# Performance work log

Measured on AMD Instinct MI355X. Metric: run time of the kernel, lower is better.

The kernel has to match this reference:

```python
import jax, jax.numpy as jnp
import numpy as np

B, T = 128, 100
NOISE_STD = 0.1  # deterministic=False path

def leaky(x, slope):
    return jnp.where(x >= 0, x, slope * x)

def setup_inputs() -> dict:
    key = jax.random.key(0)
    ks = jax.random.split(key, 24)
    s = 0.02
    d = {}
    d["input_data"] = jax.random.normal(ks[0], (B, T, 3, 3), jnp.float32)
    d["eps"] = jax.random.normal(ks[1], (B, 64), jnp.float32)
    d["noise_eps"] = jax.random.normal(ks[2], (T, B, 4), jnp.float32)
    d["proj_W"] = jax.random.normal(ks[3], (4096, 9), jnp.float32) * s
    d["proj_b"] = jnp.zeros((4096,), jnp.float32)
    d["lstm_Wih"] = jax.random.normal(ks[4], (512, 4096), jnp.float32) * s
    d["lstm_Whh"] = jax.random.normal(ks[5], (512, 128), jnp.float32) * s
    d["lstm_bih"] = jnp.zeros((512,), jnp.float32)
    d["lstm_bhh"] = jnp.zeros((512,), jnp.float32)
    d["mu_W"] = jax.random.normal(ks[6], (64, 128), jnp.float32) * s
    d["mu_b"] = jnp.zeros((64,), jnp.float32)
    d["lv_W"] = jax.random.normal(ks[7], (64, 128), jnp.float32) * s
    d["lv_b"] = jnp.zeros((64,), jnp.float32)
    d["fcin_W"] = jax.random.normal(ks[8], (256, 64), jnp.float32) * s
    d["fcin_b"] = jnp.zeros((256,), jnp.float32)
    d["gru_Wih"] = jax.random.normal(ks[9], (783, 261), jnp.float32) * s
    d["gru_Whh"] = jax.random.normal(ks[10], (783, 261), jnp.float32) * s
    d["gru_bih"] = jnp.zeros((783,), jnp.float32)
    d["gru_bhh"] = jnp.zeros((783,), jnp.float32)
    d["jf_W1"] = jax.random.normal(ks[11], (64, 261), jnp.float32) * s
    d["jf_b1"] = jnp.zeros((64,), jnp.float32)
    d["jf_W2"] = jax.random.normal(ks[12], (9, 64), jnp.float32) * s
    d["jf_b2"] = jnp.zeros((9,), jnp.float32)
    return d

def reference(input_data, eps, noise_eps, proj_W, proj_b, lstm_Wih, lstm_Whh,
              lstm_bih, lstm_bhh, mu_W, mu_b, lv_W, lv_b, fcin_W, fcin_b,
              gru_Wih, gru_Whh, gru_bih, gru_bhh, jf_W1, jf_b1, jf_W2, jf_b2):
    b, t = input_data.shape[0], input_data.shape[1]
    pose = input_data.reshape(b, t, 9)
    # pose_projection: Linear(9, 4096) + LeakyReLU(0.1)
    proj = leaky(jnp.einsum('btj,kj->btk', pose, proj_W) + proj_b, 0.1)  # (B,T,4096)

    # LSTM over time, take final hidden state. PyTorch gate order: i,f,g,o.
    # Precompute input projections for all steps.
    x_gates = jnp.einsum('btk,gk->tbg', proj, lstm_Wih) + lstm_bih + lstm_bhh  # (T,B,512)
    hdim = 128
    def lstm_step(carry, xg):
        h, c = carry
        g = xg + h @ lstm_Whh.T  # (B,512)
        i, f, gg, o = jnp.split(g, 4, axis=-1)
        i, f, o = jax.nn.sigmoid(i), jax.nn.sigmoid(f), jax.nn.sigmoid(o)
        c = f * c + i * jnp.tanh(gg)
        h = o * jnp.tanh(c)
        return (h, c), None
    h0 = jnp.zeros((b, hdim), proj.dtype)
    (h_T, _), _ = jax.lax.scan(lstm_step, (h0, h0), x_gates)

    # VAE head (dropout in eval mode = identity)
    mu = leaky(h_T @ mu_W.T + mu_b, 0.1)
    logvar = jnp.clip(leaky(h_T @ lv_W.T + lv_b, 0.1), -10.0, 10.0)
    std = jnp.exp(0.5 * logvar)
    embedding = mu + eps * std

    x = embedding @ fcin_W.T + fcin_b  # (B,256)

    # Decoder GRU loop. PyTorch gate order: r,z,n; h' = (1-z)*n + z*h.
    noise = noise_eps * NOISE_STD  # (T,B,4)
    time_steps = (jnp.arange(t, dtype=x.dtype) / (t - 1))[:, None, None] * jnp.ones((t, b, 1), x.dtype)
    inp_seq = jnp.concatenate([jnp.broadcast_to(x[None], (t, b, 256)), noise, time_steps], axis=-1)  # (T,B,261)
    gx_seq = jnp.einsum('tbk,gk->tbg', inp_seq, gru_Wih) + gru_bih  # (T,B,783)

    def gru_step(h, gx):
        gh = h @ gru_Whh.T + gru_bhh
        gx_r, gx_z, gx_n = jnp.split(gx, 3, axis=-1)
        gh_r, gh_z, gh_n = jnp.split(gh, 3, axis=-1)
        r = jax.nn.sigmoid(gx_r + gh_r)
        z = jax.nn.sigmoid(gx_z + gh_z)
        n = jnp.tanh(gx_n + r * gh_n)
        h = (1.0 - z) * n + z * h
        frame = jax.nn.sigmoid(leaky(h @ jf_W1.T + jf_b1, 0.2) @ jf_W2.T + jf_b2)
        return h, frame

    h0g = jnp.zeros((b, 261), x.dtype)
    _, frames = jax.lax.scan(gru_step, h0g, gx_seq)  # (T,B,9)
    outputs = frames.transpose(1, 0, 2).reshape(b, t, 3, 3)
    return outputs, mu, logvar
```

## Files before the change

kernel.cpp:

```cpp
#include <hip/hip_runtime.h>
#include <hip/hip_bf16.h>

typedef float f32x4 __attribute__((ext_vector_type(4)));
typedef short s16x8 __attribute__((ext_vector_type(8)));

__device__ __forceinline__ float pv_sigm(float x){ return 1.0f/(1.0f + __expf(-x)); }
__device__ __forceinline__ float pv_tanh(float x){ float e = __expf(2.0f*x); return 1.0f - 2.0f/(e + 1.0f); }

__device__ __forceinline__ unsigned short pv_f2b(float x){
  union { float f; unsigned u; } c; c.f = x;
  unsigned r = (c.u + 0x7fffu + ((c.u >> 16) & 1u)) >> 16;
  return (unsigned short)r;
}
__device__ __forceinline__ unsigned pv_pack2(float a, float b){
  return ((unsigned)pv_f2b(b) << 16) | (unsigned)pv_f2b(a);
}
__device__ __forceinline__ float pv_lo(unsigned u){
  union { unsigned u; float f; } c; c.u = u << 16; return c.f;
}
__device__ __forceinline__ float pv_hi(unsigned u){
  union { unsigned u; float f; } c; c.u = u & 0xffff0000u; return c.f;
}

__device__ __forceinline__ unsigned char pv_fp8(float x){
  union { float f; unsigned u; } c; c.f = x;
  unsigned s = (c.u >> 24) & 0x80u;
  unsigned au = c.u & 0x7fffffffu;
  if (au == 0u) return (unsigned char)s;
  int ex = (int)(au >> 23) - 127;
  if (ex < -6) ex = -6;
  union { unsigned u; float f; } iv; iv.u = (unsigned)(3 - ex + 127) << 23;
  union { unsigned u; float f; } a;  a.u = au;
  int q = (int)rintf(a.f * iv.f);
  if (q >= 16) { q >>= 1; ex += 1; }
  unsigned bits;
  if (ex == -6 && q < 8) bits = (unsigned)q;
  else bits = (unsigned)(((ex + 7) << 3) | (q - 8));
  return (unsigned char)(s | bits);
}

#if defined(__has_builtin)
#if __has_builtin(__builtin_amdgcn_cvt_pk_fp8_f32)
#define PV_HW_FP8 1
#endif
#endif
__device__ __forceinline__ unsigned char pv_fp8_fast(float x){
#ifdef PV_HW_FP8
  return (unsigned char)__builtin_amdgcn_cvt_pk_fp8_f32(x, x, 0, false);
#else
  return pv_fp8(x);
#endif
}

__global__ void pv_prep_gru8(const float* Whh, const float* Wih,
                             unsigned long long* wfp8){
  int idx = blockIdx.x*256 + threadIdx.x;
  if (idx >= 29376) return;
  int T = idx / 576;
  int rem = idx - T*576;
  int c = rem >> 6;
  int l = rem & 63;
  int l16 = l & 15;
  int quad = l >> 4;
  int jb = T / 3;
  int ty = T - jb*3;
  int j = jb*16 + l16;
  int g = ty*261 + j;
  unsigned long long v = 0ull;
  #pragma unroll
  for (int e = 0; e < 8; ++e) {
    int k = c*32 + quad*8 + e;
    float w = 0.0f;
    if (j < 261) {
      if (k < 261) w = Whh[g*261 + k];
      else if (k < 266 && ty < 2) w = Wih[g*261 + 256 + (k - 261)];
    }
    v |= (unsigned long long)pv_fp8(8.0f*w) << (8*e);
  }
  wfp8[idx] = v;
}

__global__ __launch_bounds__(256) void pv_prep_wih(
    const float* __restrict__ Wih, unsigned* __restrict__ wihb)
{
  const int idx = blockIdx.x*256 + threadIdx.x;
  if (idx >= 262144) return;
  const float* src = Wih + idx*8;
  float4 a = *(const float4*)(src);
  float4 b = *(const float4*)(src + 4);
  uint4 o;
  o.x = pv_pack2(a.x, a.y);
  o.y = pv_pack2(a.z, a.w);
  o.z = pv_pack2(b.x, b.y);
  o.w = pv_pack2(b.z, b.w);
  *(uint4*)(wihb + idx*4) = o;
}

__global__ __launch_bounds__(512, 1) void pv_gemm4(
    const float* __restrict__ pose, const float* __restrict__ projW,
    const float* __restrict__ projb, const unsigned* __restrict__ wihb,
    const float* __restrict__ bih, const float* __restrict__ bhh,
    float* __restrict__ xg)
{
  __shared__ __align__(16) unsigned As2[128*20];
  __shared__ __align__(16) unsigned Bs2[2][256*20];
  __shared__ __align__(16) float Ws2[2][320];

  const int tid = threadIdx.x;
  const int m0 = blockIdx.x * 128;
  const int n0 = blockIdx.y * 256;
  const int wave = tid >> 6, lane = tid & 63;
  const int wm = wave >> 2, wn = wave & 3;
  const int l16 = lane & 15, quad = lane >> 4;
  const int rl = tid >> 2, kq = tid & 3;
  const int rb = tid >> 1, hb = tid & 1;

  float p[9];
  {
    const float* pr = pose + (m0 + rl)*9;
    #pragma unroll
    for (int j = 0; j < 9; ++j) p[j] = pr[j];
  }

  if (tid < 320) {
    Ws2[0][tid < 288 ? ((tid >> 5)*32 + (tid & 31)) : tid] =
        (tid < 288) ? projW[(tid & 31)*9 + (tid >> 5)] : projb[tid - 288];
  }
  {
    const unsigned* src = wihb + (n0 + rb)*2048 + hb*8;
    *(uint4*)(&Bs2[0][rb*20 + hb*8])     = *(const uint4*)(src);
    *(uint4*)(&Bs2[0][rb*20 + hb*8 + 4]) = *(const uint4*)(src + 4);
  }
  __syncthreads();

  f32x4 acc[4][4];
  #pragma unroll
  for (int i = 0; i < 4; ++i)
    #pragma unroll
    for (int j = 0; j < 4; ++j) acc[i][j] = (f32x4){0.f,0.f,0.f,0.f};

  for (int kk = 0; kk < 128; ++kk) {
    const int cur = kk & 1, nxt = cur ^ 1;
    const int kn = kk + 1;

    uint4 bn0, bn1; float wv = 0.0f;
    if (kn < 128) {
      const unsigned* bsrc = wihb + (n0 + rb)*2048 + kn*16 + hb*8;
      bn0 = *(const uint4*)(bsrc);
      bn1 = *(const uint4*)(bsrc + 4);
      if (tid < 320)
        wv = (tid < 288) ? projW[kn*288 + (tid & 31)*9 + (tid >> 5)]
                         : projb[kn*32 + (tid - 288)];
    }

    {
      const float* W = Ws2[cur];
      f32x4 slo = *(const f32x4*)(W + 288 + kq*8);
      f32x4 shi = *(const f32x4*)(W + 292 + kq*8);
      #pragma unroll
      for (int j = 0; j < 9; ++j) {
        f32x4 wlo = *(const f32x4*)(W + j*32 + kq*8);
        f32x4 whi = *(const f32x4*)(W + j*32 + kq*8 + 4);
        slo += p[j]*wlo;
        shi += p[j]*whi;
      }
      #pragma unroll
      for (int e = 0; e < 4; ++e) {
        slo[e] = fmaxf(slo[e], 0.1f*slo[e]);
        shi[e] = fmaxf(shi[e], 0.1f*shi[e]);
      }
      uint4 av;
      av.x = pv_pack2(slo[0], slo[1]);
      av.y = pv_pack2(slo[2], slo[3]);
      av.z = pv_pack2(shi[0], shi[1]);
      av.w = pv_pack2(shi[2], shi[3]);
      *(uint4*)(&As2[rl*20 + kq*4]) = av;
    }
    __syncthreads();

    {
      const unsigned short* As16 = (const unsigned short*)As2;
      const unsigned short* Bs16 = (const unsigned short*)Bs2[cur];
      s16x8 af[4];
      #pragma unroll
      for (int i = 0; i < 4; ++i)
        af[i] = *(const s16x8*)(As16 + (wm*64 + i*16 + l16)*40 + quad*8);
      #pragma unroll
      for (int j = 0; j < 4; ++j) {
        s16x8 bv = *(const s16x8*)(Bs16 + (wn*64 + j*16 + l16)*40 + quad*8);
        #pragma unroll
        for (int i = 0; i < 4; ++i)
          acc[i][j] = __builtin_amdgcn_mfma_f32_16x16x32_bf16(af[i], bv, acc[i][j], 0, 0, 0);
      }
    }

    if (kn < 128) {
      *(uint4*)(&Bs2[nxt][rb*20 + hb*8])     = bn0;
      *(uint4*)(&Bs2[nxt][rb*20 + hb*8 + 4]) = bn1;
      if (tid < 320)
        Ws2[nxt][tid < 288 ? ((tid >> 5)*32 + (tid & 31)) : tid] = wv;
    }
    __syncthreads();
  }

  #pragma unroll
  for (int j = 0; j < 4; ++j) {
    int col = n0 + wn*64 + j*16 + l16;
    float bsum = bih[col] + bhh[col];
    #pragma unroll
    for (int i = 0; i < 4; ++i) {
      #pragma unroll
      for (int r = 0; r < 4; ++r) {
        int row = m0 + wm*64 + i*16 + quad*4 + r;
        int bb = row / 100;
        int tt = row - bb*100;
        xg[(tt*128 + bb)*512 + col] = acc[i][j][r] + bsum;
      }
    }
  }
}

__global__ __launch_bounds__(256) void pv_gemm(
    const float* pose, const float* projW, const float* projb,
    const float* Wih, const float* bih, const float* bhh,
    float* xg)
{
  __shared__ __align__(16) unsigned As[128*24];
  __shared__ __align__(16) unsigned Bs[128*24];
  __shared__ float Ws[320];

  const int tid = threadIdx.x;
  const int m0 = blockIdx.x * 128;
  const int n0 = blockIdx.y * 128;

  const int rl = tid >> 1;
  const int kh = tid & 1;
  float p0,p1,p2,p3,p4,p5,p6,p7,p8;
  {
    const float* pr = pose + (m0 + rl) * 9;
    p0=pr[0]; p1=pr[1]; p2=pr[2]; p3=pr[3]; p4=pr[4];
    p5=pr[5]; p6=pr[6]; p7=pr[7]; p8=pr[8];
  }

  const int wave = tid >> 6;
  const int lane = tid & 63;
  const int wm = wave >> 1, wn = wave & 1;
  const int l16 = lane & 15, quad = lane >> 4;

  f32x4 acc[4][4];
  #pragma unroll
  for (int i = 0; i < 4; ++i)
    #pragma unroll
    for (int j = 0; j < 4; ++j) acc[i][j] = (f32x4){0.f,0.f,0.f,0.f};

  for (int kk = 0; kk < 128; ++kk) {
    __syncthreads();
    for (int idx = tid; idx < 320; idx += 256)
      Ws[idx] = (idx < 288) ? projW[kk*288 + idx] : projb[kk*32 + (idx - 288)];
    #pragma unroll
    for (int i = 0; i < 8; ++i) {
      int q = tid + i*256;
      int nl = q >> 4;
      int kp = q & 15;
      const float* src = Wih + (n0 + nl)*4096 + kk*32 + kp*2;
      Bs[nl*24 + kp] = pv_pack2(src[0], src[1]);
    }
    __syncthreads();
    {
      const int kbase = kh*16;
      const float* wbase = Ws + kbase*9;
      float av[16];
      #pragma unroll
      for (int u = 0; u < 16; ++u) {
        const float* wr = wbase + u*9;
        float s = Ws[288 + kbase + u]
                + p0*wr[0] + p1*wr[1] + p2*wr[2] + p3*wr[3] + p4*wr[4]
                + p5*wr[5] + p6*wr[6] + p7*wr[7] + p8*wr[8];
        av[u] = fmaxf(s, 0.1f*s);
      }
      #pragma unroll
      for (int q = 0; q < 8; ++q)
        As[rl*24 + kh*8 + q] = pv_pack2(av[2*q], av[2*q+1]);
    }
    __syncthreads();
    const unsigned short* As16 = (const unsigned short*)As;
    const unsigned short* Bs16 = (const unsigned short*)Bs;
    s16x8 af[4], bfv[4];
    #pragma unroll
    for (int i = 0; i < 4; ++i)
      af[i] = *(const s16x8*)(As16 + (wm*64 + i*16 + l16)*48 + quad*8);
    #pragma unroll
    for (int j = 0; j < 4; ++j)
      bfv[j] = *(const s16x8*)(Bs16 + (wn*64 + j*16 + l16)*48 + quad*8);
    #pragma unroll
    for (int i = 0; i < 4; ++i)
      #pragma unroll
      for (int j = 0; j < 4; ++j)
        acc[i][j] = __builtin_amdgcn_mfma_f32_16x16x32_bf16(af[i], bfv[j], acc[i][j], 0, 0, 0);
  }
  #pragma unroll
  for (int j = 0; j < 4; ++j) {
    int col = n0 + wn*64 + j*16 + l16;
    float bsum = bih[col] + bhh[col];
    #pragma unroll
    for (int i = 0; i < 4; ++i) {
      #pragma unroll
      for (int r = 0; r < 4; ++r) {
        int row = m0 + wm*64 + i*16 + quad*4 + r;
        int bb = row / 100;
        int tt = row - bb*100;
        xg[(tt*128 + bb)*512 + col] = acc[i][j][r] + bsum;
      }
    }
  }
}

__global__ __launch_bounds__(512, 1) void pv_lstm3(
    const float* __restrict__ xg, const float* __restrict__ Whh,
    float* __restrict__ hT)
{
  __shared__ __align__(16) unsigned short Hs[16*136];
  __shared__ __align__(16) float Ds[4*512];
  const int tid = threadIdx.x;
  const int wv = tid >> 6;
  const int lane = tid & 63;
  const int l16 = lane & 15, quad = lane >> 4;
  const int m0 = blockIdx.x * 4;
  const int j = wv*16 + l16;

  s16x8 bfr[4][4];
  #pragma unroll
  for (int ty = 0; ty < 4; ++ty) {
    const int g = ty*128 + j;
    #pragma unroll
    for (int c = 0; c < 4; ++c) {
      s16x8 v;
      #pragma unroll
      for (int e = 0; e < 8; ++e)
        v[e] = (short)pv_f2b(Whh[g*128 + c*32 + quad*8 + e]);
      bfr[ty][c] = v;
    }
  }
  for (int i = tid; i < 16*136; i += 512) Hs[i] = 0;

  const int r_u = tid >> 7;
  const int j_u = tid & 127;
  float cst = 0.0f;
  const float* xbase = xg + (m0 + r_u)*512 + j_u;

  float xv[4];
  #pragma unroll
  for (int ty = 0; ty < 4; ++ty) xv[ty] = xbase[ty*128];
  __syncthreads();

  for (int t = 0; t < 100; ++t) {
    float xn[4];
    if (t < 99) {
      #pragma unroll
      for (int ty = 0; ty < 4; ++ty)
        xn[ty] = xbase[(t+1)*65536 + ty*128];
    }
    f32x4 acc[4];
    #pragma unroll
    for (int ty = 0; ty < 4; ++ty) acc[ty] = (f32x4){0.f,0.f,0.f,0.f};
    #pragma unroll
    for (int c = 0; c < 4; ++c) {
      s16x8 a = *(const s16x8*)(&Hs[l16*136 + c*32 + quad*8]);
      #pragma unroll
      for (int ty = 0; ty < 4; ++ty)
        acc[ty] = __builtin_amdgcn_mfma_f32_16x16x32_bf16(a, bfr[ty][c], acc[ty], 0, 0, 0);
    }
    if (quad == 0) {
      #pragma unroll
      for (int ty = 0; ty < 4; ++ty)
        #pragma unroll
        for (int r = 0; r < 4; ++r)
          Ds[r*512 + ty*128 + j] = acc[ty][r];
    }
    __syncthreads();

    {
      const float* dsr = Ds + r_u*512;
      float gi = dsr[j_u]       + xv[0];
      float gf = dsr[128 + j_u] + xv[1];
      float gg = dsr[256 + j_u] + xv[2];
      float go = dsr[384 + j_u] + xv[3];
      float c_ = pv_sigm(gf)*cst + pv_sigm(gi)*pv_tanh(gg);
      cst = c_;
      float h = pv_sigm(go)*pv_tanh(c_);
      Hs[r_u*136 + j_u] = pv_f2b(h);
      if (t == 99) hT[(m0 + r_u)*128 + j_u] = h;
    }
    if (t < 99) {
      #pragma unroll
      for (int ty = 0; ty < 4; ++ty) xv[ty] = xn[ty];
    }
    __syncthreads();
  }
}

__global__ __launch_bounds__(64) void pv_head(
    const float* hT, const float* eps,
    const float* muW, const float* mub,
    const float* lvW, const float* lvb,
    const float* fcW, const float* fcb,
    float* xvec, float* out)
{
  __shared__ float hrow[128];
  __shared__ float emb[64];
  const int b = blockIdx.x, j = threadIdx.x;
  hrow[j] = hT[b*128 + j];
  hrow[j + 64] = hT[b*128 + 64 + j];
  __syncthreads();
  float sm = mub[j], sl = lvb[j];
  for (int k = 0; k < 128; ++k) {
    sm += hrow[k]*muW[j*128 + k];
    sl += hrow[k]*lvW[j*128 + k];
  }
  float mu = fmaxf(sm, 0.1f*sm);
  float lv = fmaxf(sl, 0.1f*sl);
  lv = fminf(fmaxf(lv, -10.0f), 10.0f);
  float em = mu + eps[b*64 + j]*__expf(0.5f*lv);
  emb[j] = em;
  out[115200 + b*64 + j] = mu;
  out[123392 + b*64 + j] = lv;
  __syncthreads();
  for (int c4 = 0; c4 < 4; ++c4) {
    int c = c4*64 + j;
    float s = fcb[c];
    for (int k = 0; k < 64; ++k) s += emb[k]*fcW[c*64 + k];
    xvec[b*256 + c] = s;
  }
}

__global__ __launch_bounds__(256) void pv_gxbase(
    const float* xvec, const float* Wih,
    const float* bih, const float* bhh, float* gxb)
{
  __shared__ float xs[8*256];
  const int tid = threadIdx.x;
  const int bg = blockIdx.x;
  const int gg = blockIdx.y;
  for (int i = tid; i < 2048; i += 256) xs[i] = xvec[bg*2048 + i];
  __syncthreads();
  const int g = gg*256 + tid;
  if (g >= 783) return;
  float bias = bih[g] + ((g < 522) ? bhh[g] : 0.0f);
  float a0=bias,a1=bias,a2=bias,a3=bias,a4=bias,a5=bias,a6=bias,a7=bias;
  const float* wr = Wih + g*261;
  for (int k = 0; k < 256; ++k) {
    float w = wr[k];
    a0 += xs[0*256 + k]*w; a1 += xs[1*256 + k]*w;
    a2 += xs[2*256 + k]*w; a3 += xs[3*256 + k]*w;
    a4 += xs[4*256 + k]*w; a5 += xs[5*256 + k]*w;
    a6 += xs[6*256 + k]*w; a7 += xs[7*256 + k]*w;
  }
  gxb[(bg*8 + 0)*783 + g] = a0; gxb[(bg*8 + 1)*783 + g] = a1;
  gxb[(bg*8 + 2)*783 + g] = a2; gxb[(bg*8 + 3)*783 + g] = a3;
  gxb[(bg*8 + 4)*783 + g] = a4; gxb[(bg*8 + 5)*783 + g] = a5;
  gxb[(bg*8 + 6)*783 + g] = a6; gxb[(bg*8 + 7)*783 + g] = a7;
}

__global__ __launch_bounds__(512, 1) void pv_gru5(
    const float* __restrict__ gxb, const unsigned long long* __restrict__ wfp8,
    const float* __restrict__ Wih, const float* __restrict__ bhh,
    const float* __restrict__ noise, float* __restrict__ hseq)
{
  __shared__ __align__(16) unsigned long long Bl[27*9*64];
  __shared__ __align__(16) unsigned char A2[16*296];
  __shared__ __align__(16) float Ds[4*792];
  const int tid = threadIdx.x;
  const int wv = tid >> 6;
  const int lane = tid & 63;
  const int l16 = lane & 15, quad = lane >> 4;
  const int m0 = blockIdx.x * 4;
  const int tailOwner = (wv >= 5);

  long bfr[3][9];
  #pragma unroll
  for (int s = 0; s < 3; ++s)
    #pragma unroll
    for (int c = 0; c < 9; ++c)
      bfr[s][c] = (long)wfp8[((3*wv + s)*9 + c)*64 + lane];
  #pragma unroll
  for (int s = 0; s < 3; ++s)
    #pragma unroll
    for (int c = 0; c < 9; ++c)
      asm volatile("" : "+v"(bfr[s][c]));

  const int r_u = tid & 3;
  const int j1 = tid >> 2;
  const int j2 = 128 + j1;
  const int hasE3 = (tid < 20);
  const int j3 = 256 + (tid >> 2);
  float gx1[3], gx2[3], gx3[3], wn1[5], wn2[5], wn3[5];
  float bh1, bh2, bh3 = 0.f, h1 = 0.f, h2 = 0.f, h3 = 0.f;
  {
    const float* gb = gxb + (m0 + r_u)*783;
    gx1[0] = gb[j1]; gx1[1] = gb[261 + j1]; gx1[2] = gb[522 + j1];
    gx2[0] = gb[j2]; gx2[1] = gb[261 + j2]; gx2[2] = gb[522 + j2];
    const float* w1 = Wih + (522 + j1)*261 + 256;
    wn1[0] = 0.1f*w1[0]; wn1[1] = 0.1f*w1[1]; wn1[2] = 0.1f*w1[2];
    wn1[3] = 0.1f*w1[3]; wn1[4] = w1[4];
    const float* w2 = Wih + (522 + j2)*261 + 256;
    wn2[0] = 0.1f*w2[0]; wn2[1] = 0.1f*w2[1]; wn2[2] = 0.1f*w2[2];
    wn2[3] = 0.1f*w2[3]; wn2[4] = w2[4];
    bh1 = bhh[522 + j1];
    bh2 = bhh[522 + j2];
    #pragma unroll
    for (int k = 0; k < 3; ++k) gx3[k] = 0.f;
    #pragma unroll
    for (int k = 0; k < 5; ++k) wn3[k] = 0.f;
    if (hasE3) {
      gx3[0] = gb[j3]; gx3[1] = gb[261 + j3]; gx3[2] = gb[522 + j3];
      const float* w3 = Wih + (522 + j3)*261 + 256;
      wn3[0] = 0.1f*w3[0]; wn3[1] = 0.1f*w3[1]; wn3[2] = 0.1f*w3[2];
      wn3[3] = 0.1f*w3[3]; wn3[4] = w3[4];
      bh3 = bhh[522 + j3];
    }
  }

  for (int i = tid; i < 27*9*64; i += 512) Bl[i] = wfp8[24*9*64 + i];
  for (int i = tid; i < 4736; i += 512) A2[i] = 0;
  __syncthreads();
  if (tid < 20) {
    const int m = tid/5, i = tid - (tid/5)*5;
    float v = (i < 4) ? noise[(m0 + m)*4 + i]*0.1f : 0.0f;
    A2[m*296 + 261 + i] = pv_fp8(4.0f*v);
  }
  __syncthreads();

  const float inv32 = 1.0f/32.0f;
  const float* nptr = noise + (m0 + r_u)*4;
  for (int t = 0; t < 100; ++t) {
    const float4 ne = *(const float4*)(nptr + t*512);

    f32x4 acc[7];
    #pragma unroll
    for (int s = 0; s < 7; ++s) acc[s] = (f32x4){0,0,0,0};
    #pragma unroll
    for (int c = 0; c < 9; ++c) {
      const long a = *(const long*)(&A2[l16*296 + c*32 + quad*8]);
      acc[0] = __builtin_amdgcn_mfma_f32_16x16x32_fp8_fp8(a, bfr[0][c], acc[0], 0, 0, 0);
      acc[1] = __builtin_amdgcn_mfma_f32_16x16x32_fp8_fp8(a, bfr[1][c], acc[1], 0, 0, 0);
      acc[2] = __builtin_amdgcn_mfma_f32_16x16x32_fp8_fp8(a, bfr[2][c], acc[2], 0, 0, 0);
      const long b3 = (long)Bl[((3*wv + 0)*9 + c)*64 + lane];
      const long b4 = (long)Bl[((3*wv + 1)*9 + c)*64 + lane];
      const long b5 = (long)Bl[((3*wv + 2)*9 + c)*64 + lane];
      acc[3] = __builtin_amdgcn_mfma_f32_16x16x32_fp8_fp8(a, b3, acc[3], 0, 0, 0);
      acc[4] = __builtin_amdgcn_mfma_f32_16x16x32_fp8_fp8(a, b4, acc[4], 0, 0, 0);
      acc[5] = __builtin_amdgcn_mfma_f32_16x16x32_fp8_fp8(a, b5, acc[5], 0, 0, 0);
      if (tailOwner) {
        const long b6 = (long)Bl[((24 + (wv - 5))*9 + c)*64 + lane];
        acc[6] = __builtin_amdgcn_mfma_f32_16x16x32_fp8_fp8(a, b6, acc[6], 0, 0, 0);
      }
    }
    if (quad == 0) {
      #pragma unroll
      for (int s = 0; s < 3; ++s) {
        const int g = s*261 + wv*16 + l16;
        #pragma unroll
        for (int r = 0; r < 4; ++r) Ds[r*792 + g] = acc[s][r];
      }
      #pragma unroll
      for (int s = 0; s < 3; ++s) {
        const int g = s*261 + (8 + wv)*16 + l16;
        #pragma unroll
        for (int r = 0; r < 4; ++r) Ds[r*792 + g] = acc[3 + s][r];
      }
      if (tailOwner && l16 < 5) {
        const int g = (wv - 5)*261 + 256 + l16;
        #pragma unroll
        for (int r = 0; r < 4; ++r) Ds[r*792 + g] = acc[6][r];
      }
    }
    __syncthreads();

    {
      const float tv = (float)t * (1.0f/99.0f);
      const float* dsr = Ds + r_u*792;
      {
        float Dr = dsr[j1]*inv32 + gx1[0];
        float Dz = dsr[261 + j1]*inv32 + gx1[1];
        float Dn = dsr[522 + j1]*inv32;
        float nterm = ne.x*wn1[0] + ne.y*wn1[1] + ne.z*wn1[2]
                    + ne.w*wn1[3] + tv*wn1[4];
        float r_ = pv_sigm(Dr);
        float z_ = pv_sigm(Dz);
        float n_ = pv_tanh(gx1[2] + nterm + r_*(Dn + bh1));
        h1 = (1.0f - z_)*n_ + z_*h1;
        hseq[(t*128 + m0 + r_u)*261 + j1] = h1;
        A2[r_u*296 + j1] = pv_fp8_fast(4.0f*h1);
      }
      {
        float Dr = dsr[j2]*inv32 + gx2[0];
        float Dz = dsr[261 + j2]*inv32 + gx2[1];
        float Dn = dsr[522 + j2]*inv32;
        float nterm = ne.x*wn2[0] + ne.y*wn2[1] + ne.z*wn2[2]
                    + ne.w*wn2[3] + tv*wn2[4];
        float r_ = pv_sigm(Dr);
        float z_ = pv_sigm(Dz);
        float n_ = pv_tanh(gx2[2] + nterm + r_*(Dn + bh2));
        h2 = (1.0f - z_)*n_ + z_*h2;
        hseq[(t*128 + m0 + r_u)*261 + j2] = h2;
        A2[r_u*296 + j2] = pv_fp8_fast(4.0f*h2);
      }
      if (hasE3) {
        float Dr = dsr[j3]*inv32 + gx3[0];
        float Dz = dsr[261 + j3]*inv32 + gx3[1];
        float Dn = dsr[522 + j3]*inv32;
        float nterm = ne.x*wn3[0] + ne.y*wn3[1] + ne.z*wn3[2]
                    + ne.w*wn3[3] + tv*wn3[4];
        float r_ = pv_sigm(Dr);
        float z_ = pv_sigm(Dz);
        float n_ = pv_tanh(gx3[2] + nterm + r_*(Dn + bh3));
        h3 = (1.0f - z_)*n_ + z_*h3;
        hseq[(t*128 + m0 + r_u)*261 + j3] = h3;
        A2[r_u*296 + j3] = pv_fp8_fast(4.0f*h3);
      }
    }
    if (t < 99 && tid >= 40 && tid < 60) {
      const int k = tid - 40;
      const int m = k/5, i = k - (k/5)*5;
      float v = (i < 4) ? noise[((t+1)*128 + m0 + m)*4 + i]*0.1f
                        : (t+1)*(1.0f/99.0f);
      A2[m*296 + 261 + i] = pv_fp8(4.0f*v);
    }
    __syncthreads();
  }
}

__global__ __launch_bounds__(256) void pv_frames(
    const float* hseq, const float* W1, const float* b1,
    const float* W2, const float* b2, float* out)
{
  __shared__ __align__(16) float h16[16*264];
  __shared__ unsigned w1p[64*133];
  __shared__ float f1s[16*66];
  __shared__ float w2s[576];
  const int tid = threadIdx.x;
  const int r0 = blockIdx.x * 16;
  for (int i = tid; i < 16*264; i += 256) {
    int r = i / 264, k = i - r*264;
    h16[i] = (k < 261) ? hseq[(r0 + r)*261 + k] : 0.0f;
  }
  for (int i = tid; i < 64*131; i += 256) {
    int c = i/131, kp = i - (i/131)*131;
    int k = kp*2;
    float a0 = W1[c*261 + k];
    float a1 = (k + 1 < 261) ? W1[c*261 + k + 1] : 0.0f;
    w1p[c*133 + kp] = pv_pack2(a0, a1);
  }
  for (int i = tid; i < 576; i += 256) w2s[i] = W2[i];
  __syncthreads();
  #pragma unroll
  for (int e = 0; e < 4; ++e) {
    const int el = tid + e*256;
    const int r = el >> 6, c = el & 63;
    float s = b1[c];
    const unsigned* wp = w1p + c*133;
    const float* hr = h16 + r*264;
    for (int kp = 0; kp < 131; ++kp) {
      unsigned w = wp[kp];
      s += pv_lo(w)*hr[2*kp] + pv_hi(w)*hr[2*kp + 1];
    }
    f1s[r*66 + c] = fmaxf(s, 0.2f*s);
  }
  __syncthreads();
  if (tid < 144) {
    const int r = tid/9, oc = tid - (tid/9)*9;
    float s = b2[oc];
    const float* fr = f1s + r*66;
    const float* w = w2s + oc*64;
    #pragma unroll 8
    for (int k = 0; k < 64; ++k) s += fr[k]*w[k];
    const int rt = r0 + r;
    const int tt = rt >> 7, bb = rt & 127;
    out[bb*900 + tt*9 + oc] = pv_sigm(s);
  }
}

extern "C" __attribute__((visibility("default")))
void kernel_launch(void* const* d_in, const int* in_sizes, int n_in,
                   void* d_out, int out_size, void* d_ws, size_t ws_size,
                   hipStream_t stream)
{
  (void)in_sizes; (void)n_in; (void)out_size;
  const float* input_data = (const float*)d_in[0];
  const float* eps        = (const float*)d_in[1];
  const float* noise_eps  = (const float*)d_in[2];
  const float* proj_W     = (const float*)d_in[3];
  const float* proj_b     = (const float*)d_in[4];
  const float* lstm_Wih   = (const float*)d_in[5];
  const float* lstm_Whh   = (const float*)d_in[6];
  const float* lstm_bih   = (const float*)d_in[7];
  const float* lstm_bhh   = (const float*)d_in[8];
  const float* mu_W       = (const float*)d_in[9];
  const float* mu_b       = (const float*)d_in[10];
  const float* lv_W       = (const float*)d_in[11];
  const float* lv_b       = (const float*)d_in[12];
  const float* fcin_W     = (const float*)d_in[13];
  const float* fcin_b     = (const float*)d_in[14];
  const float* gru_Wih    = (const float*)d_in[15];
  const float* gru_Whh    = (const float*)d_in[16];
  const float* gru_bih    = (const float*)d_in[17];
  const float* gru_bhh    = (const float*)d_in[18];
  const float* jf_W1      = (const float*)d_in[19];
  const float* jf_b1      = (const float*)d_in[20];
  const float* jf_W2      = (const float*)d_in[21];
  const float* jf_b2      = (const float*)d_in[22];

  char* w = (char*)d_ws;
  float*              xg   = (float*)(w);
  unsigned long long* wfp8 = (unsigned long long*)(w + 26214400);
  float*              hT   = (float*)(w + 26449408);
  float*              xvec = (float*)(w + 26514944);
  float*              gxb  = (float*)(w + 26646016);
  float*              hseq = (float*)(w + 27046912);
  unsigned*           wihb = (unsigned*)(w + 40410112);
  float*              outf = (float*)d_out;

  const int use_split = (ws_size >= (size_t)44604416ull);

  pv_prep_gru8<<<115, 256, 0, stream>>>(gru_Whh, gru_Wih, wfp8);
  if (use_split) {
    pv_prep_wih<<<1024, 256, 0, stream>>>(lstm_Wih, wihb);
    pv_gemm4<<<dim3(100, 2), 512, 0, stream>>>(input_data, proj_W, proj_b, wihb,
                                               lstm_bih, lstm_bhh, xg);
  } else {
    pv_gemm<<<dim3(100, 4), 256, 0, stream>>>(input_data, proj_W, proj_b,
                                              lstm_Wih, lstm_bih, lstm_bhh, xg);
  }
  pv_lstm3<<<32, 512, 0, stream>>>(xg, lstm_Whh, hT);
  pv_head<<<128, 64, 0, stream>>>(hT, eps, mu_W, mu_b, lv_W, lv_b,
                                  fcin_W, fcin_b, xvec, outf);
  pv_gxbase<<<dim3(16, 4), 256, 0, stream>>>(xvec, gru_Wih, gru_bih, gru_bhh, gxb);
  pv_gru5<<<32, 512, 0, stream>>>(gxb, wfp8, gru_Wih, gru_bhh, noise_eps, hseq);
  pv_frames<<<800, 256, 0, stream>>>(hseq, jf_W1, jf_b1, jf_W2, jf_b2, outf);
}
```

Measured before the change: 678.7 us.

## Split the LSTM input GEMM along K into four slices and add a reduction kernel

Measured after the change: 720.7 us. 6.2% more time.

```diff
diff --git a/kernel.cpp b/kernel.cpp
--- a/kernel.cpp
+++ b/kernel.cpp
@@ -96,11 +96,10 @@
   *(uint4*)(wihb + idx*4) = o;
 }
 
-__global__ __launch_bounds__(512, 1) void pv_gemm4(
+__global__ __launch_bounds__(512, 1) void pv_gemm4k(
     const float* __restrict__ pose, const float* __restrict__ projW,
     const float* __restrict__ projb, const unsigned* __restrict__ wihb,
-    const float* __restrict__ bih, const float* __restrict__ bhh,
-    float* __restrict__ xg)
+    float* __restrict__ xg, float* __restrict__ xgp)
 {
   __shared__ __align__(16) unsigned As2[128*20];
   __shared__ __align__(16) unsigned Bs2[2][256*20];
@@ -109,6 +108,10 @@
   const int tid = threadIdx.x;
   const int m0 = blockIdx.x * 128;
   const int n0 = blockIdx.y * 256;
+  const int zz = blockIdx.z;
+  const int k0 = zz * 32;
+  float* outp = (zz == 0) ? xg : xgp + (size_t)(zz - 1)*6553600u;
+
   const int wave = tid >> 6, lane = tid & 63;
   const int wm = wave >> 2, wn = wave & 3;
   const int l16 = lane & 15, quad = lane >> 4;
@@ -124,10 +127,11 @@
 
   if (tid < 320) {
     Ws2[0][tid < 288 ? ((tid >> 5)*32 + (tid & 31)) : tid] =
-        (tid < 288) ? projW[(tid & 31)*9 + (tid >> 5)] : projb[tid - 288];
+        (tid < 288) ? projW[k0*288 + (tid & 31)*9 + (tid >> 5)]
+                    : projb[k0*32 + (tid - 288)];
   }
   {
-    const unsigned* src = wihb + (n0 + rb)*2048 + hb*8;
+    const unsigned* src = wihb + (n0 + rb)*2048 + k0*16 + hb*8;
     *(uint4*)(&Bs2[0][rb*20 + hb*8])     = *(const uint4*)(src);
     *(uint4*)(&Bs2[0][rb*20 + hb*8 + 4]) = *(const uint4*)(src + 4);
   }
@@ -139,12 +143,13 @@
     #pragma unroll
     for (int j = 0; j < 4; ++j) acc[i][j] = (f32x4){0.f,0.f,0.f,0.f};
 
-  for (int kk = 0; kk < 128; ++kk) {
+  for (int kk = k0; kk < k0 + 32; ++kk) {
     const int cur = kk & 1, nxt = cur ^ 1;
     const int kn = kk + 1;
+    const int more = (kn < k0 + 32);
 
     uint4 bn0, bn1; float wv = 0.0f;
-    if (kn < 128) {
+    if (more) {
       const unsigned* bsrc = wihb + (n0 + rb)*2048 + kn*16 + hb*8;
       bn0 = *(const uint4*)(bsrc);
       bn1 = *(const uint4*)(bsrc + 4);
@@ -194,7 +199,7 @@
       }
     }
 
-    if (kn < 128) {
+    if (more) {
       *(uint4*)(&Bs2[nxt][rb*20 + hb*8])     = bn0;
       *(uint4*)(&Bs2[nxt][rb*20 + hb*8 + 4]) = bn1;
       if (tid < 320)
@@ -206,7 +211,6 @@
   #pragma unroll
   for (int j = 0; j < 4; ++j) {
     int col = n0 + wn*64 + j*16 + l16;
-    float bsum = bih[col] + bhh[col];
     #pragma unroll
     for (int i = 0; i < 4; ++i) {
       #pragma unroll
@@ -214,10 +218,30 @@
         int row = m0 + wm*64 + i*16 + quad*4 + r;
         int bb = row / 100;
         int tt = row - bb*100;
-        xg[(tt*128 + bb)*512 + col] = acc[i][j][r] + bsum;
-      }
-    }
-  }
+        outp[(tt*128 + bb)*512 + col] = acc[i][j][r];
+      }
+    }
+  }
+}
+
+__global__ __launch_bounds__(256) void pv_xgadd(
+    float* __restrict__ xg, const float* __restrict__ xgp,
+    const float* __restrict__ bih, const float* __restrict__ bhh)
+{
+  const int i = blockIdx.x*256 + threadIdx.x;
+  float4 a = ((const float4*)xg)[i];
+  float4 b = ((const float4*)xgp)[i];
+  float4 c = ((const float4*)xgp)[1638400 + i];
+  float4 d = ((const float4*)xgp)[3276800 + i];
+  const int col4 = (i & 127)*4;
+  float4 bi = *(const float4*)(bih + col4);
+  float4 bh = *(const float4*)(bhh + col4);
+  float4 o;
+  o.x = a.x + b.x + c.x + d.x + bi.x + bh.x;
+  o.y = a.y + b.y + c.y + d.y + bi.y + bh.y;
+  o.z = a.z + b.z + c.z + d.z + bi.z + bh.z;
+  o.w = a.w + b.w + c.w + d.w + bi.w + bh.w;
+  ((float4*)xg)[i] = o;
 }
 
 __global__ __launch_bounds__(256) void pv_gemm(
@@ -718,15 +742,17 @@
   float*              gxb  = (float*)(w + 26646016);
   float*              hseq = (float*)(w + 27046912);
   unsigned*           wihb = (unsigned*)(w + 40410112);
+  float*              xgp  = (float*)(w + 44604416);
   float*              outf = (float*)d_out;
 
-  const int use_split = (ws_size >= (size_t)44604416ull);
+  const int use_split = (ws_size >= (size_t)123247616ull);
 
   pv_prep_gru8<<<115, 256, 0, stream>>>(gru_Whh, gru_Wih, wfp8);
   if (use_split) {
     pv_prep_wih<<<1024, 256, 0, stream>>>(lstm_Wih, wihb);
-    pv_gemm4<<<dim3(100, 2), 512, 0, stream>>>(input_data, proj_W, proj_b, wihb,
-                                               lstm_bih, lstm_bhh, xg);
+    pv_gemm4k<<<dim3(100, 2, 4), 512, 0, stream>>>(input_data, proj_W, proj_b,
+                                                   wihb, xg, xgp);
+    pv_xgadd<<<6400, 256, 0, stream>>>(xg, xgp, lstm_bih, lstm_bhh);
   } else {
     pv_gemm<<<dim3(100, 4), 256, 0, stream>>>(input_data, proj_W, proj_b,
                                               lstm_Wih, lstm_bih, lstm_bhh, xg);
```

## Triple-buffer GEMM B tiles and double-buffer A to drop one barrier per step

Applied to the files above, without the earlier changes.

New measurement: 671.6 us, median of 2. About the same (-1.0%).

```diff
diff --git a/kernel.cpp b/kernel.cpp
--- a/kernel.cpp
+++ b/kernel.cpp
@@ -96,15 +96,15 @@
   *(uint4*)(wihb + idx*4) = o;
 }
 
-__global__ __launch_bounds__(512, 1) void pv_gemm4(
+__global__ __launch_bounds__(512, 1) void pv_gemm5(
     const float* __restrict__ pose, const float* __restrict__ projW,
     const float* __restrict__ projb, const unsigned* __restrict__ wihb,
     const float* __restrict__ bih, const float* __restrict__ bhh,
     float* __restrict__ xg)
 {
-  __shared__ __align__(16) unsigned As2[128*20];
-  __shared__ __align__(16) unsigned Bs2[2][256*20];
-  __shared__ __align__(16) float Ws2[2][320];
+  __shared__ __align__(16) unsigned As2[2][128*20];
+  __shared__ __align__(16) unsigned Bs3[3][256*20];
+  __shared__ __align__(16) float Ws3[3][320];
 
   const int tid = threadIdx.x;
   const int m0 = blockIdx.x * 128;
@@ -122,14 +122,40 @@
     for (int j = 0; j < 9; ++j) p[j] = pr[j];
   }
 
-  if (tid < 320) {
-    Ws2[0][tid < 288 ? ((tid >> 5)*32 + (tid & 31)) : tid] =
-        (tid < 288) ? projW[(tid & 31)*9 + (tid >> 5)] : projb[tid - 288];
-  }
+  #pragma unroll
+  for (int s = 0; s < 2; ++s) {
+    if (tid < 320) {
+      Ws3[s][tid < 288 ? ((tid >> 5)*32 + (tid & 31)) : tid] =
+          (tid < 288) ? projW[s*288 + (tid & 31)*9 + (tid >> 5)]
+                      : projb[s*32 + (tid - 288)];
+    }
+    const unsigned* src = wihb + (n0 + rb)*2048 + s*16 + hb*8;
+    *(uint4*)(&Bs3[s][rb*20 + hb*8])     = *(const uint4*)(src);
+    *(uint4*)(&Bs3[s][rb*20 + hb*8 + 4]) = *(const uint4*)(src + 4);
+  }
+  __syncthreads();
   {
-    const unsigned* src = wihb + (n0 + rb)*2048 + hb*8;
-    *(uint4*)(&Bs2[0][rb*20 + hb*8])     = *(const uint4*)(src);
-    *(uint4*)(&Bs2[0][rb*20 + hb*8 + 4]) = *(const uint4*)(src + 4);
+    const float* W = Ws3[0];
+    f32x4 slo = *(const f32x4*)(W + 288 + kq*8);
+    f32x4 shi = *(const f32x4*)(W + 292 + kq*8);
+    #pragma unroll
+    for (int j = 0; j < 9; ++j) {
+      f32x4 wlo = *(const f32x4*)(W + j*32 + kq*8);
+      f32x4 whi = *(const f32x4*)(W + j*32 + kq*8 + 4);
+      slo += p[j]*wlo;
+      shi += p[j]*whi;
+    }
+    #pragma unroll
+    for (int e = 0; e < 4; ++e) {
+      slo[e] = fmaxf(slo[e], 0.1f*slo[e]);
+      shi[e] = fmaxf(shi[e], 0.1f*shi[e]);
+    }
+    uint4 av;
+    av.x = pv_pack2(slo[0], slo[1]);
+    av.y = pv_pack2(slo[2], slo[3]);
+    av.z = pv_pack2(shi[0], shi[1]);
+    av.w = pv_pack2(shi[2], shi[3]);
+    *(uint4*)(&As2[0][rl*20 + kq*4]) = av;
   }
   __syncthreads();
 
@@ -139,22 +165,23 @@
     #pragma unroll
     for (int j = 0; j < 4; ++j) acc[i][j] = (f32x4){0.f,0.f,0.f,0.f};
 
+  int b0 = 0, b1 = 1, b2 = 2;
   for (int kk = 0; kk < 128; ++kk) {
-    const int cur = kk & 1, nxt = cur ^ 1;
-    const int kn = kk + 1;
+    const int k1 = kk + 1;
+    const int k2 = kk + 2;
 
     uint4 bn0, bn1; float wv = 0.0f;
-    if (kn < 128) {
-      const unsigned* bsrc = wihb + (n0 + rb)*2048 + kn*16 + hb*8;
+    if (k2 < 128) {
+      const unsigned* bsrc = wihb + (n0 + rb)*2048 + k2*16 + hb*8;
       bn0 = *(const uint4*)(bsrc);
       bn1 = *(const uint4*)(bsrc + 4);
       if (tid < 320)
-        wv = (tid < 288) ? projW[kn*288 + (tid & 31)*9 + (tid >> 5)]
-                         : projb[kn*32 + (tid - 288)];
-    }
-
-    {
-      const float* W = Ws2[cur];
+        wv = (tid < 288) ? projW[k2*288 + (tid & 31)*9 + (tid >> 5)]
+                         : projb[k2*32 + (tid - 288)];
+    }
+
+    if (k1 < 128) {
+      const float* W = Ws3[b1];
       f32x4 slo = *(const f32x4*)(W + 288 + kq*8);
       f32x4 shi = *(const f32x4*)(W + 292 + kq*8);
       #pragma unroll
@@ -174,13 +201,12 @@
       av.y = pv_pack2(slo[2], slo[3]);
       av.z = pv_pack2(shi[0], shi[1]);
       av.w = pv_pack2(shi[2], shi[3]);
-      *(uint4*)(&As2[rl*20 + kq*4]) = av;
-    }
-    __syncthreads();
+      *(uint4*)(&As2[k1 & 1][rl*20 + kq*4]) = av;
+    }
 
     {
-      const unsigned short* As16 = (const unsigned short*)As2;
-      const unsigned short* Bs16 = (const unsigned short*)Bs2[cur];
+      const unsigned short* As16 = (const unsigned short*)As2[kk & 1];
+      const unsigned short* Bs16 = (const unsigned short*)Bs3[b0];
       s16x8 af[4];
       #pragma unroll
       for (int i = 0; i < 4; ++i)
@@ -194,13 +220,15 @@
       }
     }
 
-    if (kn < 128) {
-      *(uint4*)(&Bs2[nxt][rb*20 + hb*8])     = bn0;
-      *(uint4*)(&Bs2[nxt][rb*20 + hb*8 + 4]) = bn1;
+    if (k2 < 128) {
+      *(uint4*)(&Bs3[b2][rb*20 + hb*8])     = bn0;
+      *(uint4*)(&Bs3[b2][rb*20 + hb*8 + 4]) = bn1;
       if (tid < 320)
-        Ws2[nxt][tid < 288 ? ((tid >> 5)*32 + (tid & 31)) : tid] = wv;
+        Ws3[b2][tid < 288 ? ((tid >> 5)*32 + (tid & 31)) : tid] = wv;
     }
     __syncthreads();
+
+    const int t = b0; b0 = b1; b1 = b2; b2 = t;
   }
 
   #pragma unroll
@@ -725,7 +753,7 @@
   pv_prep_gru8<<<115, 256, 0, stream>>>(gru_Whh, gru_Wih, wfp8);
   if (use_split) {
     pv_prep_wih<<<1024, 256, 0, stream>>>(lstm_Wih, wihb);
-    pv_gemm4<<<dim3(100, 2), 512, 0, stream>>>(input_data, proj_W, proj_b, wihb,
+    pv_gemm5<<<dim3(100, 2), 512, 0, stream>>>(input_data, proj_W, proj_b, wihb,
                                                lstm_bih, lstm_bhh, xg);
   } else {
     pv_gemm<<<dim3(100, 4), 256, 0, stream>>>(input_data, proj_W, proj_b,
```
